# Kernel tuning notes

Hardware: AMD Instinct MI355X
Metric: run time of the kernel (lower is better)

Reference implementation:

```python
import jax, jax.numpy as jnp
import numpy as np

EMB = 64
N_CONS = 100000
N_VARS = 200000
N_EDGES = 2000000


def _embed(x, shift, scale, W1, b1, W2, b2):
    # PreNormLayer (affine) -> Linear -> ReLU -> Linear -> ReLU
    x = (x - shift) * scale
    x = jax.nn.relu(x @ W1 + b1)
    return jax.nn.relu(x @ W2 + b2)


def _biconv(left, right, ei0, ei1, edge_lin, tgt_idx, n_tgt, tgt_feats,
            Wl, bl, Wr, sf, Wf, bf, sp, Woa, boa, Wob, bob):
    # gather-transform: per-edge joint features [E, EMB]
    joint = (left @ Wl + bl)[ei0] + edge_lin + (right @ Wr)[ei1]
    # feature_module_final: PreNorm(scale-only) -> ReLU -> Linear
    msg = jax.nn.relu(joint * sf) @ Wf + bf
    # scatter-add to target nodes, then post-conv PreNorm(scale-only)
    agg = jax.ops.segment_sum(msg, tgt_idx, num_segments=n_tgt) * sp
    h = jax.nn.relu(jnp.concatenate([agg, tgt_feats], axis=1) @ Woa + boa)
    return h @ Wob + bob


def _forward(constraint_features, edge_features, variable_features,
             c_shift, c_scale, c_W1, c_b1, c_W2, c_b2,
             v_shift, v_scale, v_W1, v_b1, v_W2, v_b2,
             e_shift, e_scale,
             vc_Wl, vc_bl, vc_We, vc_Wr, vc_sf, vc_Wf, vc_bf, vc_sp,
             vc_Woa, vc_boa, vc_Wob, vc_bob,
             cv_Wl, cv_bl, cv_We, cv_Wr, cv_sf, cv_Wf, cv_bf, cv_sp,
             cv_Woa, cv_boa, cv_Wob, cv_bob,
             out_W1, out_b1, out_W2, edge_indices):
    ei0, ei1 = edge_indices[0], edge_indices[1]
    c = _embed(constraint_features, c_shift, c_scale, c_W1, c_b1, c_W2, c_b2)
    v = _embed(variable_features, v_shift, v_scale, v_W1, v_b1, v_W2, v_b2)
    e = (edge_features - e_shift) * e_scale  # edge embedding = PreNorm only, dim 1
    # conv_v_to_c (right_to_left=True): target = constraints via ei0
    c = jax.nn.relu(_biconv(c, v, ei0, ei1, e @ vc_We, ei0, N_CONS, c,
                            vc_Wl, vc_bl, vc_Wr, vc_sf, vc_Wf, vc_bf, vc_sp,
                            vc_Woa, vc_boa, vc_Wob, vc_bob))
    # conv_c_to_v: target = variables via ei1
    v = jax.nn.relu(_biconv(c, v, ei0, ei1, e @ cv_We, ei1, N_VARS, v,
                            cv_Wl, cv_bl, cv_Wr, cv_sf, cv_Wf, cv_bf, cv_sp,
                            cv_Woa, cv_boa, cv_Wob, cv_bob))
    out = jax.nn.relu(v @ out_W1 + out_b1) @ out_W2  # [N_VARS, 1]
    return out.reshape(1, -1)


def setup_inputs():
    key = jax.random.key(0)
    ks = iter(jax.random.split(key, 64))

    def rn(shape, s=0.1):
        return (jax.random.normal(next(ks), shape, jnp.float32) * s).astype(jnp.float32)

    d = {}
    d["constraint_features"] = rn((N_CONS, 5), 1.0)
    d["edge_features"] = rn((N_EDGES, 1), 1.0)
    d["variable_features"] = rn((N_VARS, 19), 1.0)

    def prenorm(n, pre):
        d[pre + "shift"] = rn((n,), 0.05)
        d[pre + "scale"] = jnp.ones((n,), jnp.float32) + rn((n,), 0.05)

    prenorm(5, "c_"); prenorm(19, "v_"); prenorm(1, "e_")
    for pre, nin in (("c_", 5), ("v_", 19)):
        d[pre + "W1"] = rn((nin, EMB)); d[pre + "b1"] = rn((EMB,), 0.02)
        d[pre + "W2"] = rn((EMB, EMB)); d[pre + "b2"] = rn((EMB,), 0.02)
    for pre in ("vc_", "cv_"):
        d[pre + "Wl"] = rn((EMB, EMB)); d[pre + "bl"] = rn((EMB,), 0.02)
        d[pre + "We"] = rn((1, EMB)); d[pre + "Wr"] = rn((EMB, EMB))
        d[pre + "sf"] = jnp.float32(1.0) + rn((), 0.05)
        d[pre + "Wf"] = rn((EMB, EMB)); d[pre + "bf"] = rn((EMB,), 0.02)
        d[pre + "sp"] = jnp.float32(1.0) + rn((), 0.05)
        d[pre + "Woa"] = rn((2 * EMB, EMB)); d[pre + "boa"] = rn((EMB,), 0.02)
        d[pre + "Wob"] = rn((EMB, EMB)); d[pre + "bob"] = rn((EMB,), 0.02)
    d["out_W1"] = rn((EMB, EMB)); d["out_b1"] = rn((EMB,), 0.02)
    d["out_W2"] = rn((EMB, 1))
    d["edge_indices"] = jnp.stack([
        jax.random.randint(next(ks), (N_EDGES,), 0, N_CONS),
        jax.random.randint(next(ks), (N_EDGES,), 0, N_VARS)]).astype(jnp.int32)
    d["n_cons_per_sample"] = jnp.array([N_CONS], jnp.int32)
    d["n_vars_per_sample"] = jnp.array([N_VARS], jnp.int32)
    return d


def reference(constraint_features, edge_features, variable_features,
              c_shift, c_scale, c_W1, c_b1, c_W2, c_b2,
              v_shift, v_scale, v_W1, v_b1, v_W2, v_b2,
              e_shift, e_scale,
              vc_Wl, vc_bl, vc_We, vc_Wr, vc_sf, vc_Wf, vc_bf, vc_sp,
              vc_Woa, vc_boa, vc_Wob, vc_bob,
              cv_Wl, cv_bl, cv_We, cv_Wr, cv_sf, cv_Wf, cv_bf, cv_sp,
              cv_Woa, cv_boa, cv_Wob, cv_bob,
              out_W1, out_b1, out_W2,
              edge_indices, n_cons_per_sample, n_vars_per_sample):
    return _forward(constraint_features, edge_features, variable_features,
                    c_shift, c_scale, c_W1, c_b1, c_W2, c_b2,
                    v_shift, v_scale, v_W1, v_b1, v_W2, v_b2,
                    e_shift, e_scale,
                    vc_Wl, vc_bl, vc_We, vc_Wr, vc_sf, vc_Wf, vc_bf, vc_sp,
                    vc_Woa, vc_boa, vc_Wob, vc_bob,
                    cv_Wl, cv_bl, cv_We, cv_Wr, cv_sf, cv_Wf, cv_bf, cv_sp,
                    cv_Woa, cv_boa, cv_Wob, cv_bob,
                    out_W1, out_b1, out_W2, edge_indices)
```

## Files before the change

kernel.cpp:

```cpp
#include <hip/hip_runtime.h>
#include <hip/hip_bf16.h>

#define DEV __device__ __forceinline__

typedef __attribute__((ext_vector_type(8))) short short8;
typedef __attribute__((ext_vector_type(4))) float f32x4;

DEV unsigned short f2bf(float f) {
    __hip_bfloat16 h = __float2bfloat16(f);
    unsigned short u;
    __builtin_memcpy(&u, &h, 2);
    return u;
}
DEV float bf2f(unsigned short u) { return __uint_as_float((unsigned int)u << 16); }

DEV f32x4 mfma_bf16(short8 a, short8 b, f32x4 c) {
    return __builtin_amdgcn_mfma_f32_16x16x32_bf16(a, b, c, 0, 0, 0);
}

DEV void make_hilo(const float* a8, short8& hi, short8& lo) {
    #pragma unroll
    for (int j = 0; j < 8; ++j) {
        const float v = a8[j];
        const unsigned short h = f2bf(v);
        hi[j] = (short)h;
        lo[j] = (short)f2bf(v - bf2f(h));
    }
}

DEV void mfma3(f32x4 acc[4], short8 ah, short8 al,
               const unsigned short* __restrict__ Bh,
               const unsigned short* __restrict__ Bl,
               int nkt, int tidx, int lane) {
    #pragma unroll
    for (int c = 0; c < 4; ++c) {
        const size_t o = ((size_t)(c * nkt + tidx) * 64 + lane) * 8;
        const short8 bh = *(const short8*)(Bh + o);
        const short8 bl = *(const short8*)(Bl + o);
        acc[c] = mfma_bf16(ah, bh, acc[c]);
        acc[c] = mfma_bf16(al, bh, acc[c]);
        acc[c] = mfma_bf16(ah, bl, acc[c]);
    }
}

DEV int swf(int row, int col) {
    return row * 64 + ((((col >> 3) ^ row) & 7) << 3) + (col & 7);
}

DEV void gemm_lds(f32x4 acc[4], const float* Xl,
                  const unsigned short* Bh, const unsigned short* Bl,
                  int nkt, int t0, int ntk, int l15, int q, int lane) {
    for (int t = 0; t < ntk; ++t) {
        const int ch = (t * 4 + q) ^ (l15 & 7);
        const float* a8 = Xl + l15 * 64 + ch * 8;
        short8 ah, al;
        make_hilo(a8, ah, al);
        mfma3(acc, ah, al, Bh, Bl, nkt, t0 + t, lane);
    }
}

DEV void gemm_glb(f32x4 acc[4], const float* __restrict__ Xg, int rbase, int N,
                  const unsigned short* Bh, const unsigned short* Bl,
                  int nkt, int t0, int ntk, int l15, int q, int lane) {
    const int grow = rbase + l15;
    const bool ok = grow < N;
    for (int t = 0; t < ntk; ++t) {
        float a8[8];
        if (ok) {
            const float4 v0 = *(const float4*)(Xg + (size_t)grow * 64 + t * 32 + q * 8);
            const float4 v1 = *(const float4*)(Xg + (size_t)grow * 64 + t * 32 + q * 8 + 4);
            a8[0] = v0.x; a8[1] = v0.y; a8[2] = v0.z; a8[3] = v0.w;
            a8[4] = v1.x; a8[5] = v1.y; a8[6] = v1.z; a8[7] = v1.w;
        } else {
            #pragma unroll
            for (int j = 0; j < 8; ++j) a8[j] = 0.f;
        }
        short8 ah, al;
        make_hilo(a8, ah, al);
        mfma3(acc, ah, al, Bh, Bl, nkt, t0 + t, lane);
    }
}

#define NMAT 15
struct PrepArgs {
    const float* src[NMAT];
    unsigned short* hi[NMAT];
    unsigned short* lo[NMAT];
    int nkt[NMAT];
    int KR[NMAT];
};

__global__ __launch_bounds__(256)
void prep_kernel(PrepArgs pa)
{
    const int m = blockIdx.y;
    const int nkt = pa.nkt[m];
    const int nthr = nkt * 4 * 64;
    const int p = blockIdx.x * 256 + threadIdx.x;
    if (p >= nthr) return;
    const int f = p >> 6, l = p & 63;
    const int c = f / nkt, t = f % nkt;
    const int kbase = t * 32 + ((l >> 4) << 3);
    const int n = c * 16 + (l & 15);
    const float* W = pa.src[m];
    const int KR = pa.KR[m];
    unsigned short* ph = pa.hi[m] + (size_t)p * 8;
    unsigned short* pl = pa.lo[m] + (size_t)p * 8;
    #pragma unroll
    for (int j = 0; j < 8; ++j) {
        const int k = kbase + j;
        const float v = (k < KR) ? W[k * 64 + n] : 0.f;
        const unsigned short h = f2bf(v);
        ph[j] = h;
        pl[j] = f2bf(v - bf2f(h));
    }
}

template<int IN, bool HAS_T2>
__global__ __launch_bounds__(256)
void embed_mfma(const float* __restrict__ x, int N,
                const float* __restrict__ shift, const float* __restrict__ scale,
                const unsigned short* __restrict__ W1h, const unsigned short* __restrict__ W1l,
                const float* __restrict__ b1,
                const unsigned short* __restrict__ W2h, const unsigned short* __restrict__ W2l,
                const float* __restrict__ b2,
                float* __restrict__ Em,
                const unsigned short* __restrict__ Wt1h, const unsigned short* __restrict__ Wt1l,
                const float* __restrict__ bt1, const float* __restrict__ sf1p,
                unsigned short* __restrict__ T1,
                const unsigned short* __restrict__ Wt2h, const unsigned short* __restrict__ Wt2l,
                const float* __restrict__ sf2p, unsigned short* __restrict__ T2)
{
    __shared__ __align__(16) float X0[4][16 * 32];
    __shared__ __align__(16) float Hb[4][1024];
    __shared__ __align__(16) float Eb[4][1024];

    const int w = threadIdx.x >> 6, lane = threadIdx.x & 63;
    const int l15 = lane & 15, q = lane >> 4;
    const float sf1 = sf1p[0];
    const float sf2 = HAS_T2 ? sf2p[0] : 0.f;

    const int rbase = blockIdx.x * 64 + w * 16;

    #pragma unroll
    for (int i = 0; i < 8; ++i) {
        const int p = lane + 64 * i;
        const int row = p >> 5, col = p & 31;
        const int grow = rbase + row;
        float v = 0.f;
        if (grow < N && col < IN) v = (x[(size_t)grow * IN + col] - shift[col]) * scale[col];
        X0[w][row * 32 + (((col >> 3) ^ (row & 3)) << 3) + (col & 7)] = v;
    }

    {
        f32x4 acc[4] = {{0,0,0,0},{0,0,0,0},{0,0,0,0},{0,0,0,0}};
        const int ch = q ^ (l15 & 3);
        short8 ah, al;
        make_hilo(&X0[w][l15 * 32 + ch * 8], ah, al);
        mfma3(acc, ah, al, W1h, W1l, 1, 0, lane);
        #pragma unroll
        for (int c = 0; c < 4; ++c) {
            const int col = c * 16 + l15;
            const float bb = b1[col];
            #pragma unroll
            for (int r = 0; r < 4; ++r)
                Hb[w][swf(q * 4 + r, col)] = fmaxf(acc[c][r] + bb, 0.f);
        }
    }
    {
        f32x4 acc[4] = {{0,0,0,0},{0,0,0,0},{0,0,0,0},{0,0,0,0}};
        gemm_lds(acc, Hb[w], W2h, W2l, 2, 0, 2, l15, q, lane);
        #pragma unroll
        for (int c = 0; c < 4; ++c) {
            const int col = c * 16 + l15;
            const float bb = b2[col];
            #pragma unroll
            for (int r = 0; r < 4; ++r) {
                const int row = q * 4 + r;
                const int grow = rbase + row;
                const float v = fmaxf(acc[c][r] + bb, 0.f);
                Eb[w][swf(row, col)] = v;
                if (grow < N) Em[(size_t)grow * 64 + col] = v;
            }
        }
    }
    {
        f32x4 acc[4] = {{0,0,0,0},{0,0,0,0},{0,0,0,0},{0,0,0,0}};
        gemm_lds(acc, Eb[w], Wt1h, Wt1l, 2, 0, 2, l15, q, lane);
        #pragma unroll
        for (int c = 0; c < 4; ++c) {
            const int col = c * 16 + l15;
            const float bb = bt1 ? bt1[col] : 0.f;
            #pragma unroll
            for (int r = 0; r < 4; ++r) {
                const int grow = rbase + q * 4 + r;
                if (grow < N) T1[(size_t)grow * 64 + col] = f2bf(sf1 * (acc[c][r] + bb));
            }
        }
    }
    if (HAS_T2) {
        f32x4 acc[4] = {{0,0,0,0},{0,0,0,0},{0,0,0,0},{0,0,0,0}};
        gemm_lds(acc, Eb[w], Wt2h, Wt2l, 2, 0, 2, l15, q, lane);
        #pragma unroll
        for (int c = 0; c < 4; ++c) {
            const int col = c * 16 + l15;
            #pragma unroll
            for (int r = 0; r < 4; ++r) {
                const int grow = rbase + q * 4 + r;
                if (grow < N) T2[(size_t)grow * 64 + col] = f2bf(sf2 * acc[c][r]);
            }
        }
    }
}

template<bool IS_POST2>
__global__ __launch_bounds__(256)
void post_mfma(int N, const float* __restrict__ G, const int* __restrict__ rs,
               const float* __restrict__ Em,
               const unsigned short* __restrict__ Wfh, const unsigned short* __restrict__ Wfl,
               const float* __restrict__ bfv, const float* __restrict__ spp,
               const unsigned short* __restrict__ Woah, const unsigned short* __restrict__ Woal,
               const float* __restrict__ boa,
               const unsigned short* __restrict__ Wobh, const unsigned short* __restrict__ Wobl,
               const float* __restrict__ bob,
               const unsigned short* __restrict__ W4h, const unsigned short* __restrict__ W4l,
               const float* __restrict__ b4,
               const float* __restrict__ sf2p, unsigned short* __restrict__ A2,
               const float* __restrict__ oW2, float* __restrict__ out)
{
    __shared__ __align__(16) float BA[4][1024];
    __shared__ __align__(16) float BB[4][1024];

    const int w = threadIdx.x >> 6, lane = threadIdx.x & 63;
    const int l15 = lane & 15, q = lane >> 4;
    const float sp = spp[0];
    const float sf2 = IS_POST2 ? 0.f : sf2p[0];
    const int rbase = blockIdx.x * 64 + w * 16;

    {
        f32x4 acc[4] = {{0,0,0,0},{0,0,0,0},{0,0,0,0},{0,0,0,0}};
        gemm_glb(acc, G, rbase, N, Wfh, Wfl, 2, 0, 2, l15, q, lane);
        float dgr[4];
        #pragma unroll
        for (int r = 0; r < 4; ++r) {
            const int grow = rbase + q * 4 + r;
            dgr[r] = (grow < N) ? (float)(rs[grow + 1] - rs[grow]) : 0.f;
        }
        #pragma unroll
        for (int c = 0; c < 4; ++c) {
            const int col = c * 16 + l15;
            const float bb = bfv[col];
            #pragma unroll
            for (int r = 0; r < 4; ++r)
                BA[w][swf(q * 4 + r, col)] = (acc[c][r] + dgr[r] * bb) * sp;
        }
    }
    {
        f32x4 acc[4] = {{0,0,0,0},{0,0,0,0},{0,0,0,0},{0,0,0,0}};
        gemm_lds(acc, BA[w], Woah, Woal, 4, 0, 2, l15, q, lane);
        gemm_glb(acc, Em, rbase, N, Woah, Woal, 4, 2, 2, l15, q, lane);
        #pragma unroll
        for (int c = 0; c < 4; ++c) {
            const int col = c * 16 + l15;
            const float bb = boa[col];
            #pragma unroll
            for (int r = 0; r < 4; ++r)
                BB[w][swf(q * 4 + r, col)] = fmaxf(acc[c][r] + bb, 0.f);
        }
    }
    {
        f32x4 acc[4] = {{0,0,0,0},{0,0,0,0},{0,0,0,0},{0,0,0,0}};
        gemm_lds(acc, BB[w], Wobh, Wobl, 2, 0, 2, l15, q, lane);
        #pragma unroll
        for (int c = 0; c < 4; ++c) {
            const int col = c * 16 + l15;
            const float bb = bob[col];
            #pragma unroll
            for (int r = 0; r < 4; ++r)
                BA[w][swf(q * 4 + r, col)] = fmaxf(acc[c][r] + bb, 0.f);
        }
    }
    {
        f32x4 acc[4] = {{0,0,0,0},{0,0,0,0},{0,0,0,0},{0,0,0,0}};
        gemm_lds(acc, BA[w], W4h, W4l, 2, 0, 2, l15, q, lane);
        if (!IS_POST2) {
            #pragma unroll
            for (int c = 0; c < 4; ++c) {
                const int col = c * 16 + l15;
                const float bb = b4[col];
                #pragma unroll
                for (int r = 0; r < 4; ++r) {
                    const int grow = rbase + q * 4 + r;
                    if (grow < N) A2[(size_t)grow * 64 + col] = f2bf(sf2 * (acc[c][r] + bb));
                }
            }
        } else {
            float w2c[4], bb4[4];
            #pragma unroll
            for (int c = 0; c < 4; ++c) {
                const int col = c * 16 + l15;
                w2c[c] = oW2[col];
                bb4[c] = b4[col];
            }
            #pragma unroll
            for (int r = 0; r < 4; ++r) {
                float s = 0.f;
                #pragma unroll
                for (int c = 0; c < 4; ++c)
                    s += fmaxf(acc[c][r] + bb4[c], 0.f) * w2c[c];
                s += __shfl_xor(s, 1);
                s += __shfl_xor(s, 2);
                s += __shfl_xor(s, 4);
                s += __shfl_xor(s, 8);
                const int grow = rbase + q * 4 + r;
                if (l15 == 0 && grow < N) out[grow] = s;
            }
        }
    }
}

__global__ __launch_bounds__(256)
void hist_rank_kernel(const int* __restrict__ ei, int E,
                      int* __restrict__ h1, int* __restrict__ h2,
                      unsigned int* __restrict__ rank)
{
    const int e = blockIdx.x * 256 + threadIdx.x;
    if (e >= E) return;
    const int r1 = atomicAdd(h1 + ei[e], 1);
    const int r2 = atomicAdd(h2 + ei[E + e], 1);
    rank[e] = (unsigned int)r1 | ((unsigned int)r2 << 16);
}

__global__ __launch_bounds__(256)
void scanA_kernel(const int* __restrict__ h, int n, int* __restrict__ csum)
{
    __shared__ int wsum[4];
    const int t = threadIdx.x, lane = t & 63, wid = t >> 6;
    const int base = blockIdx.x * 4096 + t * 16;
    int s = 0;
    #pragma unroll
    for (int j = 0; j < 16; ++j) {
        const int idx = base + j;
        if (idx < n) s += h[idx];
    }
    #pragma unroll
    for (int d = 1; d < 64; d <<= 1) s += __shfl_xor(s, d);
    if (lane == 0) wsum[wid] = s;
    __syncthreads();
    if (t == 0) csum[blockIdx.x] = wsum[0] + wsum[1] + wsum[2] + wsum[3];
}

__global__ __launch_bounds__(256)
void scanB_kernel(int* __restrict__ csum, int nchunks, int* __restrict__ rs, int n)
{
    __shared__ int wsum[4];
    const int t = threadIdx.x, lane = t & 63, wid = t >> 6;
    const int v = (t < nchunks) ? csum[t] : 0;
    int x = v;
    #pragma unroll
    for (int d = 1; d < 64; d <<= 1) { int y = __shfl_up(x, d); if (lane >= d) x += y; }
    if (lane == 63) wsum[wid] = x;
    __syncthreads();
    int woff = 0;
    for (int i = 0; i < wid; ++i) woff += wsum[i];
    if (t < nchunks) csum[t] = woff + x - v;
    if (t == 0) rs[n] = wsum[0] + wsum[1] + wsum[2] + wsum[3];
}

__global__ __launch_bounds__(256)
void scanC_kernel(const int* __restrict__ h, int n, const int* __restrict__ csum,
                  int* __restrict__ rs)
{
    __shared__ int wsum[4];
    const int t = threadIdx.x, lane = t & 63, wid = t >> 6;
    const int base = blockIdx.x * 4096 + t * 16;
    int loc[16];
    int s = 0;
    #pragma unroll
    for (int j = 0; j < 16; ++j) {
        loc[j] = s;
        const int idx = base + j;
        if (idx < n) s += h[idx];
    }
    int x = s;
    #pragma unroll
    for (int d = 1; d < 64; d <<= 1) { int y = __shfl_up(x, d); if (lane >= d) x += y; }
    if (lane == 63) wsum[wid] = x;
    __syncthreads();
    int woff = 0;
    for (int i = 0; i < wid; ++i) woff += wsum[i];
    const int toff = csum[blockIdx.x] + woff + x - s;
    #pragma unroll
    for (int j = 0; j < 16; ++j) {
        const int idx = base + j;
        if (idx < n) rs[idx] = toff + loc[j];
    }
}

__global__ __launch_bounds__(256)
void scatter_kernel(const int* __restrict__ ei, int E,
                    const float* __restrict__ ef,
                    const float* __restrict__ eshp, const float* __restrict__ escp,
                    const unsigned int* __restrict__ rank,
                    const int* __restrict__ rs1, const int* __restrict__ rs2,
                    int2* __restrict__ pairs1, int2* __restrict__ pairs2)
{
    const int e = blockIdx.x * 256 + threadIdx.x;
    if (e >= E) return;
    const int i0 = ei[e];
    const int i1 = ei[E + e];
    const unsigned int rk = rank[e];
    const float en = (ef[e] - eshp[0]) * escp[0];
    const int enb = __float_as_int(en);
    const int pos1 = rs1[i0] + (int)(rk & 0xffffu);
    const int pos2 = rs2[i1] + (int)(rk >> 16);
    pairs1[pos1] = make_int2(i1, enb);
    pairs2[pos2] = make_int2(i0, enb);
}

__global__ __launch_bounds__(256)
void agg_kernel(int nrows, const int* __restrict__ rs,
                const int2* __restrict__ pairs,
                const unsigned short* __restrict__ Ttgt,
                const unsigned short* __restrict__ Tsrc,
                const float* __restrict__ We, const float* __restrict__ sfp,
                float* __restrict__ G)
{
    const int r = threadIdx.x >> 6;
    const int j = threadIdx.x & 63;
    const int row = blockIdx.x * 4 + r;
    if (row >= nrows) return;

    const float base = bf2f(Ttgt[(size_t)row * 64 + j]);
    const float sfWe = sfp[0] * We[j];
    const int s = rs[row];
    const int e = rs[row + 1];

    float acc = 0.f;
    int p = s;
    for (; p + 1 < e; p += 2) {
        const int2 pr0 = pairs[p];
        const int2 pr1 = pairs[p + 1];
        const float bs0 = bf2f(Tsrc[(size_t)pr0.x * 64 + j]);
        const float bs1 = bf2f(Tsrc[(size_t)pr1.x * 64 + j]);
        acc += fmaxf(base + bs0 + __int_as_float(pr0.y) * sfWe, 0.f);
        acc += fmaxf(base + bs1 + __int_as_float(pr1.y) * sfWe, 0.f);
    }
    if (p < e) {
        const int2 pr = pairs[p];
        const float bs = bf2f(Tsrc[(size_t)pr.x * 64 + j]);
        acc += fmaxf(base + bs + __int_as_float(pr.y) * sfWe, 0.f);
    }
    G[(size_t)row * 64 + j] = acc;
}

extern "C" void kernel_launch(void* const* d_in, const int* in_sizes, int n_in,
                              void* d_out, int out_size, void* d_ws, size_t ws_size,
                              hipStream_t stream)
{
    const float* cf      = (const float*)d_in[0];
    const float* ef      = (const float*)d_in[1];
    const float* vf      = (const float*)d_in[2];
    const float* c_shift = (const float*)d_in[3];
    const float* c_scale = (const float*)d_in[4];
    const float* v_shift = (const float*)d_in[5];
    const float* v_scale = (const float*)d_in[6];
    const float* e_shift = (const float*)d_in[7];
    const float* e_scale = (const float*)d_in[8];
    const float* c_W1 = (const float*)d_in[9];
    const float* c_b1 = (const float*)d_in[10];
    const float* c_W2 = (const float*)d_in[11];
    const float* c_b2 = (const float*)d_in[12];
    const float* v_W1 = (const float*)d_in[13];
    const float* v_b1 = (const float*)d_in[14];
    const float* v_W2 = (const float*)d_in[15];
    const float* v_b2 = (const float*)d_in[16];
    const float* vc_Wl  = (const float*)d_in[17];
    const float* vc_bl  = (const float*)d_in[18];
    const float* vc_We  = (const float*)d_in[19];
    const float* vc_Wr  = (const float*)d_in[20];
    const float* vc_sf  = (const float*)d_in[21];
    const float* vc_Wf  = (const float*)d_in[22];
    const float* vc_bf  = (const float*)d_in[23];
    const float* vc_sp  = (const float*)d_in[24];
    const float* vc_Woa = (const float*)d_in[25];
    const float* vc_boa = (const float*)d_in[26];
    const float* vc_Wob = (const float*)d_in[27];
    const float* vc_bob = (const float*)d_in[28];
    const float* cv_Wl  = (const float*)d_in[29];
    const float* cv_bl  = (const float*)d_in[30];
    const float* cv_We  = (const float*)d_in[31];
    const float* cv_Wr  = (const float*)d_in[32];
    const float* cv_sf  = (const float*)d_in[33];
    const float* cv_Wf  = (const float*)d_in[34];
    const float* cv_bf  = (const float*)d_in[35];
    const float* cv_sp  = (const float*)d_in[36];
    const float* cv_Woa = (const float*)d_in[37];
    const float* cv_boa = (const float*)d_in[38];
    const float* cv_Wob = (const float*)d_in[39];
    const float* cv_bob = (const float*)d_in[40];
    const float* out_W1 = (const float*)d_in[41];
    const float* out_b1 = (const float*)d_in[42];
    const float* out_W2 = (const float*)d_in[43];
    const int*   eidx   = (const int*)d_in[44];

    const int NC = in_sizes[0] / 5;
    const int NV = in_sizes[2] / 19;
    const int E  = in_sizes[1];

    char* ws = (char*)d_ws;
    size_t off = 0;
    auto alloc = [&](size_t bytes) -> size_t {
        size_t o = off;
        off = (off + bytes + 255) & ~(size_t)255;
        return o;
    };
    size_t o_h1 = alloc((size_t)NC * 4);
    size_t o_h2 = alloc((size_t)NV * 4);
    size_t zero_bytes = off;
    size_t o_rs1  = alloc((size_t)(NC + 1) * 4);
    size_t o_rs2  = alloc((size_t)(NV + 1) * 4);
    size_t o_cs1  = alloc(256 * 4);
    size_t o_cs2  = alloc(256 * 4);
    size_t o_p1   = alloc((size_t)E * 8);
    size_t o_p2   = alloc((size_t)E * 8);
    size_t o_G1   = alloc((size_t)NC * 64 * 4);
    size_t o_G2   = alloc((size_t)NV * 64 * 4);
    size_t o_Emc  = alloc((size_t)NC * 64 * 4);
    size_t o_Emv  = alloc((size_t)NV * 64 * 4);
    size_t o_A1   = alloc((size_t)NC * 64 * 2);
    size_t o_B1   = alloc((size_t)NV * 64 * 2);
    size_t o_B2   = alloc((size_t)NV * 64 * 2);

    static const int nkt_arr[NMAT] = {1,2,2,1,2,2,2,2,4,2,2,2,4,2,2};
    static const int KR_arr[NMAT]  = {5,64,64,19,64,64,64,64,128,64,64,64,128,64,64};
    const float* src_arr[NMAT] = {c_W1, c_W2, vc_Wl, v_W1, v_W2, vc_Wr, cv_Wr,
                                  vc_Wf, vc_Woa, vc_Wob, cv_Wl,
                                  cv_Wf, cv_Woa, cv_Wob, out_W1};
    size_t o_wh[NMAT], o_wl[NMAT];
    for (int m = 0; m < NMAT; ++m) {
        o_wh[m] = alloc((size_t)nkt_arr[m] * 4 * 64 * 8 * 2);
        o_wl[m] = alloc((size_t)nkt_arr[m] * 4 * 64 * 8 * 2);
    }
    (void)ws_size; (void)n_in; (void)out_size;

    int*  h1   = (int*)(ws + o_h1);
    int*  h2   = (int*)(ws + o_h2);
    int*  rs1  = (int*)(ws + o_rs1);
    int*  rs2  = (int*)(ws + o_rs2);
    int*  cs1  = (int*)(ws + o_cs1);
    int*  cs2  = (int*)(ws + o_cs2);
    unsigned int* rank = (unsigned int*)(ws + o_G1);
    int2* p1   = (int2*)(ws + o_p1);
    int2* p2   = (int2*)(ws + o_p2);
    float* G1  = (float*)(ws + o_G1);
    float* G2  = (float*)(ws + o_G2);
    float* Emc = (float*)(ws + o_Emc);
    float* Emv = (float*)(ws + o_Emv);
    unsigned short* A1 = (unsigned short*)(ws + o_A1);
    unsigned short* B1 = (unsigned short*)(ws + o_B1);
    unsigned short* A2 = (unsigned short*)(ws + o_A1);
    unsigned short* B2 = (unsigned short*)(ws + o_B2);

    PrepArgs pa;
    for (int m = 0; m < NMAT; ++m) {
        pa.src[m] = src_arr[m];
        pa.hi[m] = (unsigned short*)(ws + o_wh[m]);
        pa.lo[m] = (unsigned short*)(ws + o_wl[m]);
        pa.nkt[m] = nkt_arr[m];
        pa.KR[m] = KR_arr[m];
    }
    auto WH = [&](int m) { return (const unsigned short*)(ws + o_wh[m]); };
    auto WL = [&](int m) { return (const unsigned short*)(ws + o_wl[m]); };

    hipMemsetAsync(ws, 0, zero_bytes, stream);

    prep_kernel<<<dim3(4, NMAT), 256, 0, stream>>>(pa);

    const int nch1 = (NC + 4095) / 4096, nch2 = (NV + 4095) / 4096;
    hist_rank_kernel<<<(E + 255) / 256, 256, 0, stream>>>(eidx, E, h1, h2, rank);
    scanA_kernel<<<nch1, 256, 0, stream>>>(h1, NC, cs1);
    scanB_kernel<<<1, 256, 0, stream>>>(cs1, nch1, rs1, NC);
    scanC_kernel<<<nch1, 256, 0, stream>>>(h1, NC, cs1, rs1);
    scanA_kernel<<<nch2, 256, 0, stream>>>(h2, NV, cs2);
    scanB_kernel<<<1, 256, 0, stream>>>(cs2, nch2, rs2, NV);
    scanC_kernel<<<nch2, 256, 0, stream>>>(h2, NV, cs2, rs2);
    scatter_kernel<<<(E + 255) / 256, 256, 0, stream>>>(
        eidx, E, ef, e_shift, e_scale, rank, rs1, rs2, p1, p2);

    const int tC = (NC + 63) >> 6, tV = (NV + 63) >> 6;
    embed_mfma<5, false><<<tC, 256, 0, stream>>>(
        cf, NC, c_shift, c_scale,
        WH(0), WL(0), c_b1, WH(1), WL(1), c_b2, Emc,
        WH(2), WL(2), vc_bl, vc_sf, A1,
        nullptr, nullptr, nullptr, nullptr);
    embed_mfma<19, true><<<tV, 256, 0, stream>>>(
        vf, NV, v_shift, v_scale,
        WH(3), WL(3), v_b1, WH(4), WL(4), v_b2, Emv,
        WH(5), WL(5), nullptr, vc_sf, B1,
        WH(6), WL(6), cv_sf, B2);

    agg_kernel<<<(NC + 3) / 4, 256, 0, stream>>>(
        NC, rs1, p1, A1, B1, vc_We, vc_sf, G1);
    post_mfma<false><<<tC, 256, 0, stream>>>(
        NC, G1, rs1, Emc,
        WH(7), WL(7), vc_bf, vc_sp,
        WH(8), WL(8), vc_boa,
        WH(9), WL(9), vc_bob,
        WH(10), WL(10), cv_bl,
        cv_sf, A2, nullptr, nullptr);

    agg_kernel<<<(NV + 3) / 4, 256, 0, stream>>>(
        NV, rs2, p2, B2, A2, cv_We, cv_sf, G2);
    post_mfma<true><<<tV, 256, 0, stream>>>(
        NV, G2, rs2, Emv,
        WH(11), WL(11), cv_bf, cv_sp,
        WH(12), WL(12), cv_boa,
        WH(13), WL(13), cv_bob,
        WH(14), WL(14), out_b1,
        nullptr, nullptr, out_W2, (float*)d_out);
}
```

Before: 862.9 us.

## Fuse histogram/rank with node embeddings in one kernel and batch scan launches

Merges the edge histogram/rank atomics and the two node-embedding MFMA kernels into a single launch whose blocks alternate between the atomic histogram work and embedding tiles, so the memory-bound atomics overlap with compute-bound embedding. The three-stage prefix scans for both index arrays are combined into paired launches via a grid y-dimension, cutting the scan launches from six to three. Template specialisation on input width and T2 presence is replaced by runtime selection, which may cost registers and unrolling in the embedding path. LDS is now allocated for histogram blocks too, which can limit occupancy.

```diff
diff --git a/kernel.cpp b/kernel.cpp
--- a/kernel.cpp
+++ b/kernel.cpp
@@ -116,31 +116,68 @@
     }
 }
 
-template<int IN, bool HAS_T2>
-__global__ __launch_bounds__(256)
-void embed_mfma(const float* __restrict__ x, int N,
-                const float* __restrict__ shift, const float* __restrict__ scale,
-                const unsigned short* __restrict__ W1h, const unsigned short* __restrict__ W1l,
-                const float* __restrict__ b1,
-                const unsigned short* __restrict__ W2h, const unsigned short* __restrict__ W2l,
-                const float* __restrict__ b2,
-                float* __restrict__ Em,
-                const unsigned short* __restrict__ Wt1h, const unsigned short* __restrict__ Wt1l,
-                const float* __restrict__ bt1, const float* __restrict__ sf1p,
-                unsigned short* __restrict__ T1,
-                const unsigned short* __restrict__ Wt2h, const unsigned short* __restrict__ Wt2l,
-                const float* __restrict__ sf2p, unsigned short* __restrict__ T2)
+struct FusedArgs {
+    const int* ei; int E; int nH;
+    int* h1; int* h2; unsigned int* rank;
+    int tC, tV;
+    const float* cf; int NC;
+    const float* c_shift; const float* c_scale;
+    const float* vf; int NV;
+    const float* v_shift; const float* v_scale;
+    const unsigned short *cW1h, *cW1l, *cW2h, *cW2l, *cWt1h, *cWt1l;
+    const unsigned short *vW1h, *vW1l, *vW2h, *vW2l, *vWt1h, *vWt1l, *vWt2h, *vWt2l;
+    const float *c_b1, *c_b2, *v_b1, *v_b2, *vc_bl;
+    const float *vc_sf, *cv_sf;
+    float* Emc; float* Emv;
+    unsigned short* A1; unsigned short* B1; unsigned short* B2;
+};
+
+__global__ __launch_bounds__(256)
+void fused_he_kernel(FusedArgs a)
 {
     __shared__ __align__(16) float X0[4][16 * 32];
     __shared__ __align__(16) float Hb[4][1024];
     __shared__ __align__(16) float Eb[4][1024];
 
+    const int half = blockIdx.x & 1;
+    const int idx  = blockIdx.x >> 1;
+
+    if (half == 0) {
+        const int stride = a.nH * 256;
+        for (int e = idx * 256 + (int)threadIdx.x; e < a.E; e += stride) {
+            const int r1 = atomicAdd(a.h1 + a.ei[e], 1);
+            const int r2 = atomicAdd(a.h2 + a.ei[a.E + e], 1);
+            a.rank[e] = (unsigned int)r1 | ((unsigned int)r2 << 16);
+        }
+        return;
+    }
+
+    int tile = idx;
+    const float* x; int N; int IN;
+    const float *shift, *scale, *b1, *b2, *bt1;
+    const unsigned short *W1h, *W1l, *W2h, *W2l, *Wt1h, *Wt1l;
+    const unsigned short *Wt2h = nullptr, *Wt2l = nullptr;
+    float* Em; unsigned short* T1; unsigned short* T2 = nullptr;
+    float sf1, sf2 = 0.f;
+    if (tile < a.tC) {
+        x = a.cf; N = a.NC; IN = 5; shift = a.c_shift; scale = a.c_scale;
+        W1h = a.cW1h; W1l = a.cW1l; b1 = a.c_b1;
+        W2h = a.cW2h; W2l = a.cW2l; b2 = a.c_b2;
+        Em = a.Emc; Wt1h = a.cWt1h; Wt1l = a.cWt1l; bt1 = a.vc_bl;
+        sf1 = a.vc_sf[0]; T1 = a.A1;
+    } else {
+        tile -= a.tC;
+        x = a.vf; N = a.NV; IN = 19; shift = a.v_shift; scale = a.v_scale;
+        W1h = a.vW1h; W1l = a.vW1l; b1 = a.v_b1;
+        W2h = a.vW2h; W2l = a.vW2l; b2 = a.v_b2;
+        Em = a.Emv; Wt1h = a.vWt1h; Wt1l = a.vWt1l; bt1 = nullptr;
+        sf1 = a.vc_sf[0]; T1 = a.B1;
+        Wt2h = a.vWt2h; Wt2l = a.vWt2l; sf2 = a.cv_sf[0]; T2 = a.B2;
+    }
+
     const int w = threadIdx.x >> 6, lane = threadIdx.x & 63;
     const int l15 = lane & 15, q = lane >> 4;
-    const float sf1 = sf1p[0];
-    const float sf2 = HAS_T2 ? sf2p[0] : 0.f;
-
-    const int rbase = blockIdx.x * 64 + w * 16;
+    const int rbase = tile * 64 + w * 16;
 
     #pragma unroll
     for (int i = 0; i < 8; ++i) {
@@ -198,7 +235,7 @@
             }
         }
     }
-    if (HAS_T2) {
+    if (T2 != nullptr) {
         f32x4 acc[4] = {{0,0,0,0},{0,0,0,0},{0,0,0,0},{0,0,0,0}};
         gemm_lds(acc, Eb[w], Wt2h, Wt2l, 2, 0, 2, l15, q, lane);
         #pragma unroll
@@ -320,21 +357,16 @@
 }
 
 __global__ __launch_bounds__(256)
-void hist_rank_kernel(const int* __restrict__ ei, int E,
-                      int* __restrict__ h1, int* __restrict__ h2,
-                      unsigned int* __restrict__ rank)
-{
-    const int e = blockIdx.x * 256 + threadIdx.x;
-    if (e >= E) return;
-    const int r1 = atomicAdd(h1 + ei[e], 1);
-    const int r2 = atomicAdd(h2 + ei[E + e], 1);
-    rank[e] = (unsigned int)r1 | ((unsigned int)r2 << 16);
-}
-
-__global__ __launch_bounds__(256)
-void scanA_kernel(const int* __restrict__ h, int n, int* __restrict__ csum)
+void scanA2_kernel(const int* __restrict__ h1, int n1, int* __restrict__ cs1,
+                   const int* __restrict__ h2, int n2, int* __restrict__ cs2)
 {
     __shared__ int wsum[4];
+    const int which = blockIdx.y;
+    const int* h = which ? h2 : h1;
+    const int n = which ? n2 : n1;
+    int* csum = which ? cs2 : cs1;
+    if (blockIdx.x * 4096 >= n) return;
+
     const int t = threadIdx.x, lane = t & 63, wid = t >> 6;
     const int base = blockIdx.x * 4096 + t * 16;
     int s = 0;
@@ -351,9 +383,16 @@
 }
 
 __global__ __launch_bounds__(256)
-void scanB_kernel(int* __restrict__ csum, int nchunks, int* __restrict__ rs, int n)
+void scanB2_kernel(int* __restrict__ cs1, int nch1, int* __restrict__ rs1, int n1,
+                   int* __restrict__ cs2, int nch2, int* __restrict__ rs2, int n2)
 {
     __shared__ int wsum[4];
+    const int which = blockIdx.x;
+    int* csum = which ? cs2 : cs1;
+    const int nchunks = which ? nch2 : nch1;
+    int* rs = which ? rs2 : rs1;
+    const int n = which ? n2 : n1;
+
     const int t = threadIdx.x, lane = t & 63, wid = t >> 6;
     const int v = (t < nchunks) ? csum[t] : 0;
     int x = v;
@@ -368,10 +407,19 @@
 }
 
 __global__ __launch_bounds__(256)
-void scanC_kernel(const int* __restrict__ h, int n, const int* __restrict__ csum,
-                  int* __restrict__ rs)
+void scanC2_kernel(const int* __restrict__ h1, int n1, const int* __restrict__ cs1,
+                   int* __restrict__ rs1,
+                   const int* __restrict__ h2, int n2, const int* __restrict__ cs2,
+                   int* __restrict__ rs2)
 {
     __shared__ int wsum[4];
+    const int which = blockIdx.y;
+    const int* h = which ? h2 : h1;
+    const int n = which ? n2 : n1;
+    const int* csum = which ? cs2 : cs1;
+    int* rs = which ? rs2 : rs1;
+    if (blockIdx.x * 4096 >= n) return;
+
     const int t = threadIdx.x, lane = t & 63, wid = t >> 6;
     const int base = blockIdx.x * 4096 + t * 16;
     int loc[16];
@@ -577,28 +625,31 @@
 
     prep_kernel<<<dim3(4, NMAT), 256, 0, stream>>>(pa);
 
+    const int tC = (NC + 63) >> 6, tV = (NV + 63) >> 6;
+    const int nE = tC + tV;
+    FusedArgs fa;
+    fa.ei = eidx; fa.E = E; fa.nH = nE;
+    fa.h1 = h1; fa.h2 = h2; fa.rank = rank;
+    fa.tC = tC; fa.tV = tV;
+    fa.cf = cf; fa.NC = NC; fa.c_shift = c_shift; fa.c_scale = c_scale;
+    fa.vf = vf; fa.NV = NV; fa.v_shift = v_shift; fa.v_scale = v_scale;
+    fa.cW1h = WH(0); fa.cW1l = WL(0); fa.cW2h = WH(1); fa.cW2l = WL(1);
+    fa.cWt1h = WH(2); fa.cWt1l = WL(2);
+    fa.vW1h = WH(3); fa.vW1l = WL(3); fa.vW2h = WH(4); fa.vW2l = WL(4);
+    fa.vWt1h = WH(5); fa.vWt1l = WL(5); fa.vWt2h = WH(6); fa.vWt2l = WL(6);
+    fa.c_b1 = c_b1; fa.c_b2 = c_b2; fa.v_b1 = v_b1; fa.v_b2 = v_b2;
+    fa.vc_bl = vc_bl; fa.vc_sf = vc_sf; fa.cv_sf = cv_sf;
+    fa.Emc = Emc; fa.Emv = Emv; fa.A1 = A1; fa.B1 = B1; fa.B2 = B2;
+    fused_he_kernel<<<2 * nE, 256, 0, stream>>>(fa);
+
     const int nch1 = (NC + 4095) / 4096, nch2 = (NV + 4095) / 4096;
-    hist_rank_kernel<<<(E + 255) / 256, 256, 0, stream>>>(eidx, E, h1, h2, rank);
-    scanA_kernel<<<nch1, 256, 0, stream>>>(h1, NC, cs1);
-    scanB_kernel<<<1, 256, 0, stream>>>(cs1, nch1, rs1, NC);
-    scanC_kernel<<<nch1, 256, 0, stream>>>(h1, NC, cs1, rs1);
-    scanA_kernel<<<nch2, 256, 0, stream>>>(h2, NV, cs2);
-    scanB_kernel<<<1, 256, 0, stream>>>(cs2, nch2, rs2, NV);
-    scanC_kernel<<<nch2, 256, 0, stream>>>(h2, NV, cs2, rs2);
+    const int nchm = nch1 > nch2 ? nch1 : nch2;
+    scanA2_kernel<<<dim3(nchm, 2), 256, 0, stream>>>(h1, NC, cs1, h2, NV, cs2);
+    scanB2_kernel<<<2, 256, 0, stream>>>(cs1, nch1, rs1, NC, cs2, nch2, rs2, NV);
+    scanC2_kernel<<<dim3(nchm, 2), 256, 0, stream>>>(h1, NC, cs1, rs1, h2, NV, cs2, rs2);
+
     scatter_kernel<<<(E + 255) / 256, 256, 0, stream>>>(
         eidx, E, ef, e_shift, e_scale, rank, rs1, rs2, p1, p2);
-
-    const int tC = (NC + 63) >> 6, tV = (NV + 63) >> 6;
-    embed_mfma<5, false><<<tC, 256, 0, stream>>>(
-        cf, NC, c_shift, c_scale,
-        WH(0), WL(0), c_b1, WH(1), WL(1), c_b2, Emc,
-        WH(2), WL(2), vc_bl, vc_sf, A1,
-        nullptr, nullptr, nullptr, nullptr);
-    embed_mfma<19, true><<<tV, 256, 0, stream>>>(
-        vf, NV, v_shift, v_scale,
-        WH(3), WL(3), v_b1, WH(4), WL(4), v_b2, Emv,
-        WH(5), WL(5), nullptr, vc_sf, B1,
-        WH(6), WL(6), cv_sf, B2);
 
     agg_kernel<<<(NC + 3) / 4, 256, 0, stream>>>(
         NC, rs1, p1, A1, B1, vc_We, vc_sf, G1);
```

Result: faster. 813.3 us (-5.7%).
